# Kernel optimization log

Hardware: AMD Instinct MI355X
Metric: run time of the kernel (lower is better)

## Reference

```python
import jax, jax.numpy as jnp
import numpy as np

LOSS_WEIGHT = 1.0  # init kwarg
B = 16   # number of segments
S = 2048 # points per segment (uniform; offsets are cumulative multiples of S)


def setup_inputs() -> dict:
    key = jax.random.key(0)
    k1, k2, k3, k4 = jax.random.split(key, 4)
    coord = jax.random.normal(k1, (B * S, 3), dtype=jnp.float32)
    coord_transformed = jax.random.normal(k2, (B * S, 3), dtype=jnp.float32)
    R = jax.random.normal(k3, (B, 3, 3), dtype=jnp.float32)
    t = jax.random.normal(k4, (B, 3), dtype=jnp.float32)
    offset = (jnp.arange(B, dtype=jnp.int64) + 1) * S          # cumulative end offsets
    offset_trans = (jnp.arange(B, dtype=jnp.int64) + 1) * S
    return {"coord": coord, "coord_transformed": coord_transformed,
            "R": R, "t": t, "offset": offset, "offset_trans": offset_trans}


def reference(coord, coord_transformed, R, t, offset, offset_trans):
    # Uniform segments: reshape ragged-by-offset layout to [B, S, 3].
    b = R.shape[0]
    s = coord.shape[0] // b
    src = coord.reshape(b, s, 3)
    tgt = coord_transformed.reshape(b, -1, 3)
    # Per-segment rigid transform: (Ri @ src.T).T + ti
    src_t = jnp.einsum('bij,bnj->bni', R, src) + t[:, None, :]
    # Squared pairwise distances [B, S, S] (min of dist then square == min of sq-dist).
    d2 = (jnp.sum(src_t * src_t, axis=-1)[:, :, None]
          + jnp.sum(tgt * tgt, axis=-1)[:, None, :]
          - 2.0 * jnp.einsum('bnd,bmd->bnm', src_t, tgt))
    nn_d2 = jnp.min(jnp.maximum(d2, 0.0), axis=2)  # [B, S] NN squared distance
    per_seg = jnp.mean(nn_d2, axis=1)              # reduction='mean' within segment
    loss = jnp.mean(per_seg)                       # reduction='mean' over segments
    return loss * LOSS_WEIGHT
```

## Files before the change

### kernel.cpp

```cpp
#include <hip/hip_runtime.h>
#include <math.h>


#define THREADS 512
#define NW 8
#define P 2
#define SRC_BLK 128

__global__ __launch_bounds__(THREADS)
void nn_full_kernel(const float* __restrict__ coord,
                    const float* __restrict__ coord_t,
                    const float* __restrict__ Rm,
                    const float* __restrict__ tv,
                    float* __restrict__ ws,
                    int S, int NSC) {
    extern __shared__ char smem_raw[];
    float4* tile = (float4*)smem_raw;
    float*  part = (float*)(smem_raw + (size_t)S * 16);
    float*  wsum = part + NW * 64 * P;

    const int tid  = threadIdx.x;
    const int bid  = blockIdx.x;
    const int b    = bid / NSC;
    const int sc   = bid - b * NSC;
    const int w    = tid >> 6;
    const int lane = tid & 63;

    {
        const float* tb = coord_t + (size_t)b * S * 3;
        for (int base = tid * 4; base < S; base += THREADS * 4) {
            const float4* g4 = reinterpret_cast<const float4*>(tb + (size_t)base * 3);
            const float4 q0 = g4[0], q1 = g4[1], q2 = g4[2];
            const float px[4] = {q0.x, q0.w, q1.z, q2.y};
            const float py[4] = {q0.y, q1.x, q1.w, q2.z};
            const float pz[4] = {q0.z, q1.y, q2.x, q2.w};
            #pragma unroll
            for (int k = 0; k < 4; ++k) {
                const float x = px[k], y = py[k], z = pz[k];
                tile[base + k] = make_float4(-2.f*x, -2.f*y, -2.f*z,
                                             x*x + y*y + z*z);
            }
        }
    }

    const float* Rb = Rm + (size_t)b * 9;
    const float r00=Rb[0], r01=Rb[1], r02=Rb[2];
    const float r10=Rb[3], r11=Rb[4], r12=Rb[5];
    const float r20=Rb[6], r21=Rb[7], r22=Rb[8];
    const float t0=tv[3*b], t1=tv[3*b+1], t2=tv[3*b+2];

    float TX[P], TY[P], TZ[P], SN[P], best[P];
    {
        const float* sp = coord + ((size_t)b * S + (size_t)sc * SRC_BLK + lane * P) * 3;
        #pragma unroll
        for (int j = 0; j < P; ++j) {
            const float x = sp[3*j], y = sp[3*j+1], z = sp[3*j+2];
            const float sx = __builtin_fmaf(r00,x,__builtin_fmaf(r01,y,__builtin_fmaf(r02,z,t0)));
            const float sy = __builtin_fmaf(r10,x,__builtin_fmaf(r11,y,__builtin_fmaf(r12,z,t1)));
            const float sz = __builtin_fmaf(r20,x,__builtin_fmaf(r21,y,__builtin_fmaf(r22,z,t2)));
            TX[j]=sx; TY[j]=sy; TZ[j]=sz;
            SN[j]=sx*sx + sy*sy + sz*sz;
            best[j] = 3.0e38f;
        }
    }

    __syncthreads();

    const int mPer  = S / NW;
    const int mbase = w * mPer;
    #pragma unroll 2
    for (int it = 0; it < mPer / 4; ++it) {
        const float4 p0 = tile[mbase + 4*it + 0];
        const float4 p1 = tile[mbase + 4*it + 1];
        const float4 p2 = tile[mbase + 4*it + 2];
        const float4 p3 = tile[mbase + 4*it + 3];
        #pragma unroll
        for (int j = 0; j < P; ++j) {
            const float v0 = __builtin_fmaf(p0.x,TX[j],__builtin_fmaf(p0.y,TY[j],__builtin_fmaf(p0.z,TZ[j],p0.w)));
            const float v1 = __builtin_fmaf(p1.x,TX[j],__builtin_fmaf(p1.y,TY[j],__builtin_fmaf(p1.z,TZ[j],p1.w)));
            const float v2 = __builtin_fmaf(p2.x,TX[j],__builtin_fmaf(p2.y,TY[j],__builtin_fmaf(p2.z,TZ[j],p2.w)));
            const float v3 = __builtin_fmaf(p3.x,TX[j],__builtin_fmaf(p3.y,TY[j],__builtin_fmaf(p3.z,TZ[j],p3.w)));
            best[j] = fminf(fminf(best[j], v0), v1);
            best[j] = fminf(fminf(best[j], v2), v3);
        }
    }

    #pragma unroll
    for (int j = 0; j < P; ++j)
        part[(w * 64 + lane) * P + j] = best[j] + SN[j];
    __syncthreads();

    float v = 0.0f;
    if (tid < SRC_BLK) {
        float mn = part[tid];
        #pragma unroll
        for (int ww = 1; ww < NW; ++ww)
            mn = fminf(mn, part[ww * SRC_BLK + tid]);
        v = fmaxf(mn, 0.0f);
    }
    if (tid < 128) {
        #pragma unroll
        for (int off = 32; off > 0; off >>= 1) v += __shfl_down(v, off, 64);
        if ((tid & 63) == 0) wsum[tid >> 6] = v;
    }
    __syncthreads();
    if (tid == 0) ws[bid] = wsum[0] + wsum[1];
}

__global__ __launch_bounds__(256)
void final_kernel(const float* __restrict__ partial, int n,
                  float* __restrict__ out, float scale) {
    float v = (threadIdx.x < n) ? partial[threadIdx.x] : 0.0f;
    #pragma unroll
    for (int off = 32; off > 0; off >>= 1) v += __shfl_down(v, off, 64);
    __shared__ float sm[4];
    if ((threadIdx.x & 63) == 0) sm[threadIdx.x >> 6] = v;
    __syncthreads();
    if (threadIdx.x == 0) out[0] = (sm[0] + sm[1] + sm[2] + sm[3]) * scale;
}

extern "C" void kernel_launch(void* const* d_in, const int* in_sizes, int n_in,
                              void* d_out, int out_size, void* d_ws, size_t ws_size,
                              hipStream_t stream) {
    const float* coord   = (const float*)d_in[0];
    const float* coord_t = (const float*)d_in[1];
    const float* Rm      = (const float*)d_in[2];
    const float* tv      = (const float*)d_in[3];

    const int B = in_sizes[2] / 9;
    const int S = in_sizes[0] / (3 * B);
    const int NSC = S / SRC_BLK;
    const int nblk = B * NSC;

    float* ws  = (float*)d_ws;
    float* out = (float*)d_out;

    const size_t smem = (size_t)S * 16 + NW * 64 * P * 4 + 2 * 4;

    nn_full_kernel<<<nblk, THREADS, smem, stream>>>(
        coord, coord_t, Rm, tv, ws, S, NSC);

    final_kernel<<<1, 256, 0, stream>>>(
        ws, nblk, out, 1.0f / ((float)B * (float)S));
}
```

Before: 14.32 us.

## Split target set across two blocks and raise per-thread source points

Each block now scans only half of the segment's target points (TSPLIT=2) and handles 256 source points with 4 per thread instead of 128 with 2. Every block writes per-source partial minima to workspace, and a single 1024-thread combine kernel takes the min of the two halves, clamps at zero and sums. The aim is more register reuse of each shared-memory tile load and a smaller static shared tile. The cost is an extra global round trip of 2·B·S floats through one serial reduction block, and the tile is now hardcoded at 1024 entries, which ties it to S≤2048.

```diff
diff --git a/kernel.cpp b/kernel.cpp
--- a/kernel.cpp
+++ b/kernel.cpp
@@ -4,31 +4,33 @@
 
 #define THREADS 512
 #define NW 8
-#define P 2
-#define SRC_BLK 128
+#define P 4
+#define SRC_BLK 256
+#define TSPLIT 2
 
 __global__ __launch_bounds__(THREADS)
-void nn_full_kernel(const float* __restrict__ coord,
+void nn_half_kernel(const float* __restrict__ coord,
                     const float* __restrict__ coord_t,
                     const float* __restrict__ Rm,
                     const float* __restrict__ tv,
-                    float* __restrict__ ws,
-                    int S, int NSC) {
-    extern __shared__ char smem_raw[];
-    float4* tile = (float4*)smem_raw;
-    float*  part = (float*)(smem_raw + (size_t)S * 16);
-    float*  wsum = part + NW * 64 * P;
+                    float* __restrict__ slice_min,
+                    int S, int NSC, int BS) {
+    __shared__ float4 tile[1024];
+    __shared__ float  part[NW * SRC_BLK];
 
     const int tid  = threadIdx.x;
     const int bid  = blockIdx.x;
-    const int b    = bid / NSC;
-    const int sc   = bid - b * NSC;
+    const int b    = bid / (NSC * TSPLIT);
+    const int rem  = bid - b * (NSC * TSPLIT);
+    const int sc   = rem / TSPLIT;
+    const int ts   = rem - sc * TSPLIT;
     const int w    = tid >> 6;
     const int lane = tid & 63;
+    const int halfS = S / TSPLIT;
 
     {
-        const float* tb = coord_t + (size_t)b * S * 3;
-        for (int base = tid * 4; base < S; base += THREADS * 4) {
+        const float* tb = coord_t + ((size_t)b * S + (size_t)ts * halfS) * 3;
+        for (int base = tid * 4; base < halfS; base += THREADS * 4) {
             const float4* g4 = reinterpret_cast<const float4*>(tb + (size_t)base * 3);
             const float4 q0 = g4[0], q1 = g4[1], q2 = g4[2];
             const float px[4] = {q0.x, q0.w, q1.z, q2.y};
@@ -51,10 +53,14 @@
 
     float TX[P], TY[P], TZ[P], SN[P], best[P];
     {
-        const float* sp = coord + ((size_t)b * S + (size_t)sc * SRC_BLK + lane * P) * 3;
+        const float4* g4 = reinterpret_cast<const float4*>(
+            coord + ((size_t)b * S + (size_t)sc * SRC_BLK + lane * P) * 3);
+        const float4 q0 = g4[0], q1 = g4[1], q2 = g4[2];
+        const float f[12] = {q0.x,q0.y,q0.z,q0.w, q1.x,q1.y,q1.z,q1.w,
+                             q2.x,q2.y,q2.z,q2.w};
         #pragma unroll
         for (int j = 0; j < P; ++j) {
-            const float x = sp[3*j], y = sp[3*j+1], z = sp[3*j+2];
+            const float x = f[3*j], y = f[3*j+1], z = f[3*j+2];
             const float sx = __builtin_fmaf(r00,x,__builtin_fmaf(r01,y,__builtin_fmaf(r02,z,t0)));
             const float sy = __builtin_fmaf(r10,x,__builtin_fmaf(r11,y,__builtin_fmaf(r12,z,t1)));
             const float sz = __builtin_fmaf(r20,x,__builtin_fmaf(r21,y,__builtin_fmaf(r22,z,t2)));
@@ -66,10 +72,9 @@
 
     __syncthreads();
 
-    const int mPer  = S / NW;
-    const int mbase = w * mPer;
+    const int mbase = w * (halfS / NW);
     #pragma unroll 2
-    for (int it = 0; it < mPer / 4; ++it) {
+    for (int it = 0; it < (halfS / NW) / 4; ++it) {
         const float4 p0 = tile[mbase + 4*it + 0];
         const float4 p1 = tile[mbase + 4*it + 1];
         const float4 p2 = tile[mbase + 4*it + 2];
@@ -87,36 +92,46 @@
 
     #pragma unroll
     for (int j = 0; j < P; ++j)
-        part[(w * 64 + lane) * P + j] = best[j] + SN[j];
+        part[w * SRC_BLK + lane * P + j] = best[j] + SN[j];
     __syncthreads();
 
-    float v = 0.0f;
     if (tid < SRC_BLK) {
         float mn = part[tid];
         #pragma unroll
         for (int ww = 1; ww < NW; ++ww)
             mn = fminf(mn, part[ww * SRC_BLK + tid]);
-        v = fmaxf(mn, 0.0f);
+        slice_min[(size_t)ts * BS + (size_t)b * S + (size_t)sc * SRC_BLK + tid] = mn;
     }
-    if (tid < 128) {
-        #pragma unroll
-        for (int off = 32; off > 0; off >>= 1) v += __shfl_down(v, off, 64);
-        if ((tid & 63) == 0) wsum[tid >> 6] = v;
-    }
-    __syncthreads();
-    if (tid == 0) ws[bid] = wsum[0] + wsum[1];
 }
 
-__global__ __launch_bounds__(256)
-void final_kernel(const float* __restrict__ partial, int n,
-                  float* __restrict__ out, float scale) {
-    float v = (threadIdx.x < n) ? partial[threadIdx.x] : 0.0f;
+__global__ __launch_bounds__(1024)
+void combine_final_kernel(const float* __restrict__ slice_min,
+                          float* __restrict__ out, int BS, float scale) {
+    __shared__ float sm[16];
+    const float4* s0 = reinterpret_cast<const float4*>(slice_min);
+    const float4* s1 = reinterpret_cast<const float4*>(slice_min + BS);
+    const int n4 = BS / 4;
+
+    float acc = 0.0f;
+    for (int i = threadIdx.x; i < n4; i += 1024) {
+        const float4 a = s0[i];
+        const float4 c = s1[i];
+        const float m0 = fmaxf(fminf(a.x, c.x), 0.0f);
+        const float m1 = fmaxf(fminf(a.y, c.y), 0.0f);
+        const float m2 = fmaxf(fminf(a.z, c.z), 0.0f);
+        const float m3 = fmaxf(fminf(a.w, c.w), 0.0f);
+        acc += (m0 + m1) + (m2 + m3);
+    }
     #pragma unroll
-    for (int off = 32; off > 0; off >>= 1) v += __shfl_down(v, off, 64);
-    __shared__ float sm[4];
-    if ((threadIdx.x & 63) == 0) sm[threadIdx.x >> 6] = v;
+    for (int off = 32; off > 0; off >>= 1) acc += __shfl_down(acc, off, 64);
+    if ((threadIdx.x & 63) == 0) sm[threadIdx.x >> 6] = acc;
     __syncthreads();
-    if (threadIdx.x == 0) out[0] = (sm[0] + sm[1] + sm[2] + sm[3]) * scale;
+    if (threadIdx.x == 0) {
+        float tot = 0.0f;
+        #pragma unroll
+        for (int i = 0; i < 16; ++i) tot += sm[i];
+        out[0] = tot * scale;
+    }
 }
 
 extern "C" void kernel_launch(void* const* d_in, const int* in_sizes, int n_in,
@@ -129,17 +144,16 @@
 
     const int B = in_sizes[2] / 9;
     const int S = in_sizes[0] / (3 * B);
+    const int BS = B * S;
     const int NSC = S / SRC_BLK;
-    const int nblk = B * NSC;
+    const int nblk = B * NSC * TSPLIT;
 
-    float* ws  = (float*)d_ws;
+    float* slice_min = (float*)d_ws;
     float* out = (float*)d_out;
 
-    const size_t smem = (size_t)S * 16 + NW * 64 * P * 4 + 2 * 4;
+    nn_half_kernel<<<nblk, THREADS, 0, stream>>>(
+        coord, coord_t, Rm, tv, slice_min, S, NSC, BS);
 
-    nn_full_kernel<<<nblk, THREADS, smem, stream>>>(
-        coord, coord_t, Rm, tv, ws, S, NSC);
-
-    final_kernel<<<1, 256, 0, stream>>>(
-        ws, nblk, out, 1.0f / ((float)B * (float)S));
+    combine_final_kernel<<<1, 1024, 0, stream>>>(
+        slice_min, out, BS, 1.0f / (float)BS);
 }
```

After: 16.39 us. 14.5% more time.

## Stream target points via wave-uniform scalar loads instead of LDS tile

Applied to the files above, without the earlier changes.

Removes the shared-memory staging of the target segment and the barrier that follows it. Each wave now reads its slice of target points directly from global memory with a wave-uniform address (readfirstlane), so the loads can become scalar loads, and it computes the target norms inline. The -2 factor is folded into the source coordinates instead. This saves LDS traffic and the sync, and the smaller LDS footprint may raise occupancy. In exchange every block recomputes the target norms, which adds ALU work per pair, and the scalar load path must keep pace with the math.

```diff
diff --git a/kernel.cpp b/kernel.cpp
--- a/kernel.cpp
+++ b/kernel.cpp
@@ -6,6 +6,7 @@
 #define NW 8
 #define P 2
 #define SRC_BLK 128
+#define CHUNK 16
 
 __global__ __launch_bounds__(THREADS)
 void nn_full_kernel(const float* __restrict__ coord,
@@ -14,34 +15,14 @@
                     const float* __restrict__ tv,
                     float* __restrict__ ws,
                     int S, int NSC) {
-    extern __shared__ char smem_raw[];
-    float4* tile = (float4*)smem_raw;
-    float*  part = (float*)(smem_raw + (size_t)S * 16);
-    float*  wsum = part + NW * 64 * P;
+    __shared__ float part[NW * 64 * P];
+    __shared__ float wsum[2];
 
     const int tid  = threadIdx.x;
     const int bid  = blockIdx.x;
     const int b    = bid / NSC;
     const int sc   = bid - b * NSC;
-    const int w    = tid >> 6;
     const int lane = tid & 63;
-
-    {
-        const float* tb = coord_t + (size_t)b * S * 3;
-        for (int base = tid * 4; base < S; base += THREADS * 4) {
-            const float4* g4 = reinterpret_cast<const float4*>(tb + (size_t)base * 3);
-            const float4 q0 = g4[0], q1 = g4[1], q2 = g4[2];
-            const float px[4] = {q0.x, q0.w, q1.z, q2.y};
-            const float py[4] = {q0.y, q1.x, q1.w, q2.z};
-            const float pz[4] = {q0.z, q1.y, q2.x, q2.w};
-            #pragma unroll
-            for (int k = 0; k < 4; ++k) {
-                const float x = px[k], y = py[k], z = pz[k];
-                tile[base + k] = make_float4(-2.f*x, -2.f*y, -2.f*z,
-                                             x*x + y*y + z*z);
-            }
-        }
-    }
 
     const float* Rb = Rm + (size_t)b * 9;
     const float r00=Rb[0], r01=Rb[1], r02=Rb[2];
@@ -49,7 +30,7 @@
     const float r20=Rb[6], r21=Rb[7], r22=Rb[8];
     const float t0=tv[3*b], t1=tv[3*b+1], t2=tv[3*b+2];
 
-    float TX[P], TY[P], TZ[P], SN[P], best[P];
+    float TXp[P], TYp[P], TZp[P], SN[P], best[P];
     {
         const float* sp = coord + ((size_t)b * S + (size_t)sc * SRC_BLK + lane * P) * 3;
         #pragma unroll
@@ -58,36 +39,50 @@
             const float sx = __builtin_fmaf(r00,x,__builtin_fmaf(r01,y,__builtin_fmaf(r02,z,t0)));
             const float sy = __builtin_fmaf(r10,x,__builtin_fmaf(r11,y,__builtin_fmaf(r12,z,t1)));
             const float sz = __builtin_fmaf(r20,x,__builtin_fmaf(r21,y,__builtin_fmaf(r22,z,t2)));
-            TX[j]=sx; TY[j]=sy; TZ[j]=sz;
-            SN[j]=sx*sx + sy*sy + sz*sz;
+            TXp[j] = -2.0f * sx;  TYp[j] = -2.0f * sy;  TZp[j] = -2.0f * sz;
+            SN[j]  = sx*sx + sy*sy + sz*sz;
             best[j] = 3.0e38f;
         }
     }
 
-    __syncthreads();
+    const int w_u = __builtin_amdgcn_readfirstlane(tid >> 6);
+    const int mPer = S / NW;
+    const float* tb = coord_t + ((size_t)b * S + (size_t)w_u * mPer) * 3;
 
-    const int mPer  = S / NW;
-    const int mbase = w * mPer;
-    #pragma unroll 2
-    for (int it = 0; it < mPer / 4; ++it) {
-        const float4 p0 = tile[mbase + 4*it + 0];
-        const float4 p1 = tile[mbase + 4*it + 1];
-        const float4 p2 = tile[mbase + 4*it + 2];
-        const float4 p3 = tile[mbase + 4*it + 3];
+    for (int c = 0; c < mPer / CHUNK; ++c) {
+        const float* cb = tb + c * (CHUNK * 3);
+        float f[CHUNK * 3];
         #pragma unroll
-        for (int j = 0; j < P; ++j) {
-            const float v0 = __builtin_fmaf(p0.x,TX[j],__builtin_fmaf(p0.y,TY[j],__builtin_fmaf(p0.z,TZ[j],p0.w)));
-            const float v1 = __builtin_fmaf(p1.x,TX[j],__builtin_fmaf(p1.y,TY[j],__builtin_fmaf(p1.z,TZ[j],p1.w)));
-            const float v2 = __builtin_fmaf(p2.x,TX[j],__builtin_fmaf(p2.y,TY[j],__builtin_fmaf(p2.z,TZ[j],p2.w)));
-            const float v3 = __builtin_fmaf(p3.x,TX[j],__builtin_fmaf(p3.y,TY[j],__builtin_fmaf(p3.z,TZ[j],p3.w)));
-            best[j] = fminf(fminf(best[j], v0), v1);
-            best[j] = fminf(fminf(best[j], v2), v3);
+        for (int k = 0; k < CHUNK * 3; ++k) f[k] = cb[k];
+
+        #pragma unroll
+        for (int t = 0; t < CHUNK; t += 2) {
+            const float tx0 = f[3*t+0], ty0 = f[3*t+1], tz0 = f[3*t+2];
+            const float tx1 = f[3*t+3], ty1 = f[3*t+4], tz1 = f[3*t+5];
+            const float tn0 = __builtin_fmaf(tz0, tz0,
+                              __builtin_fmaf(ty0, ty0, tx0 * tx0));
+            const float tn1 = __builtin_fmaf(tz1, tz1,
+                              __builtin_fmaf(ty1, ty1, tx1 * tx1));
+            const float a00 = __builtin_fmaf(tx0, TXp[0],
+                              __builtin_fmaf(ty0, TYp[0],
+                              __builtin_fmaf(tz0, TZp[0], tn0)));
+            const float a01 = __builtin_fmaf(tx1, TXp[0],
+                              __builtin_fmaf(ty1, TYp[0],
+                              __builtin_fmaf(tz1, TZp[0], tn1)));
+            const float a10 = __builtin_fmaf(tx0, TXp[1],
+                              __builtin_fmaf(ty0, TYp[1],
+                              __builtin_fmaf(tz0, TZp[1], tn0)));
+            const float a11 = __builtin_fmaf(tx1, TXp[1],
+                              __builtin_fmaf(ty1, TYp[1],
+                              __builtin_fmaf(tz1, TZp[1], tn1)));
+            best[0] = fminf(fminf(best[0], a00), a01);
+            best[1] = fminf(fminf(best[1], a10), a11);
         }
     }
 
     #pragma unroll
     for (int j = 0; j < P; ++j)
-        part[(w * 64 + lane) * P + j] = best[j] + SN[j];
+        part[tid * P + j] = best[j] + SN[j];
     __syncthreads();
 
     float v = 0.0f;
@@ -135,9 +130,7 @@
     float* ws  = (float*)d_ws;
     float* out = (float*)d_out;
 
-    const size_t smem = (size_t)S * 16 + NW * 64 * P * 4 + 2 * 4;
-
-    nn_full_kernel<<<nblk, THREADS, smem, stream>>>(
+    nn_full_kernel<<<nblk, THREADS, 0, stream>>>(
         coord, coord_t, Rm, tv, ws, S, NSC);
 
     final_kernel<<<1, 256, 0, stream>>>(
```

After: 18.20 us. 27.1% more time.

## Compute pairwise distance dot products with fp16 MFMA using hi/lo split

Applied to the files above, without the earlier changes.

Replaces the scalar FMA inner loop with 32x32x16 f16 MFMA instructions. Source coordinates are split into high and low fp16 parts, and the target norm is packed into the B fragment so a single matrix multiply yields -2·s·t + |t|². The min is then taken over MFMA outputs and reduced with shuffles and LDS. This moves the O(S²) work onto the matrix cores, at the cost of precision: target coordinates are only fp16 and shared memory is now fixed at 2048 entries.

```diff
diff --git a/kernel.cpp b/kernel.cpp
--- a/kernel.cpp
+++ b/kernel.cpp
@@ -4,20 +4,31 @@
 
 #define THREADS 512
 #define NW 8
-#define P 2
 #define SRC_BLK 128
+#define PART_STRIDE 18
+
+typedef __attribute__((ext_vector_type(8))) _Float16 half8;
+typedef __attribute__((ext_vector_type(16))) float f32x16;
+
+__device__ __forceinline__ unsigned short f16b(float x) {
+    _Float16 hv = (_Float16)x;
+    return __builtin_bit_cast(unsigned short, hv);
+}
+__device__ __forceinline__ float f16tof(unsigned short u) {
+    return (float)__builtin_bit_cast(_Float16, u);
+}
 
 __global__ __launch_bounds__(THREADS)
-void nn_full_kernel(const float* __restrict__ coord,
+void nn_mfma_kernel(const float* __restrict__ coord,
                     const float* __restrict__ coord_t,
                     const float* __restrict__ Rm,
                     const float* __restrict__ tv,
                     float* __restrict__ ws,
                     int S, int NSC) {
-    extern __shared__ char smem_raw[];
-    float4* tile = (float4*)smem_raw;
-    float*  part = (float*)(smem_raw + (size_t)S * 16);
-    float*  wsum = part + NW * 64 * P;
+    __shared__ uint4 Bfrag[2048];
+    __shared__ float part[128 * PART_STRIDE];
+    __shared__ float SN_lds[128];
+    __shared__ float wsum[2];
 
     const int tid  = threadIdx.x;
     const int bid  = blockIdx.x;
@@ -25,83 +36,96 @@
     const int sc   = bid - b * NSC;
     const int w    = tid >> 6;
     const int lane = tid & 63;
+    const int col  = lane & 31;
+    const int kh   = lane >> 5;
+    const int wsrc = w >> 1;
+    const int h    = w & 1;
 
     {
         const float* tb = coord_t + (size_t)b * S * 3;
-        for (int base = tid * 4; base < S; base += THREADS * 4) {
-            const float4* g4 = reinterpret_cast<const float4*>(tb + (size_t)base * 3);
-            const float4 q0 = g4[0], q1 = g4[1], q2 = g4[2];
-            const float px[4] = {q0.x, q0.w, q1.z, q2.y};
-            const float py[4] = {q0.y, q1.x, q1.w, q2.z};
-            const float pz[4] = {q0.z, q1.y, q2.x, q2.w};
-            #pragma unroll
-            for (int k = 0; k < 4; ++k) {
-                const float x = px[k], y = py[k], z = pz[k];
-                tile[base + k] = make_float4(-2.f*x, -2.f*y, -2.f*z,
-                                             x*x + y*y + z*z);
-            }
+        for (int g = tid; g < S; g += THREADS) {
+            const float tx = tb[3*g], ty = tb[3*g+1], tz = tb[3*g+2];
+            const float TN = __builtin_fmaf(tz, tz, __builtin_fmaf(ty, ty, tx*tx));
+            const unsigned uhx = f16b(-2.f*tx), uhy = f16b(-2.f*ty), uhz = f16b(-2.f*tz);
+            const unsigned TNh = f16b(TN);
+            const unsigned TNl = f16b(TN - f16tof((unsigned short)TNh));
+            uint4 wv;
+            wv.x = uhx | (uhy << 16);
+            wv.y = uhz | (uhx << 16);
+            wv.z = uhy | (uhz << 16);
+            wv.w = TNh | (TNl << 16);
+            Bfrag[g] = wv;
         }
     }
 
-    const float* Rb = Rm + (size_t)b * 9;
-    const float r00=Rb[0], r01=Rb[1], r02=Rb[2];
-    const float r10=Rb[3], r11=Rb[4], r12=Rb[5];
-    const float r20=Rb[6], r21=Rb[7], r22=Rb[8];
-    const float t0=tv[3*b], t1=tv[3*b+1], t2=tv[3*b+2];
+    half8 afrag;
+    #pragma unroll
+    for (int i = 0; i < 8; ++i) afrag[i] = (_Float16)0.0f;
+    {
+        const float* Rb = Rm + (size_t)b * 9;
+        const float r00=Rb[0], r01=Rb[1], r02=Rb[2];
+        const float r10=Rb[3], r11=Rb[4], r12=Rb[5];
+        const float r20=Rb[6], r21=Rb[7], r22=Rb[8];
+        const float t0=tv[3*b], t1=tv[3*b+1], t2=tv[3*b+2];
 
-    float TX[P], TY[P], TZ[P], SN[P], best[P];
-    {
-        const float* sp = coord + ((size_t)b * S + (size_t)sc * SRC_BLK + lane * P) * 3;
-        #pragma unroll
-        for (int j = 0; j < P; ++j) {
-            const float x = sp[3*j], y = sp[3*j+1], z = sp[3*j+2];
-            const float sx = __builtin_fmaf(r00,x,__builtin_fmaf(r01,y,__builtin_fmaf(r02,z,t0)));
-            const float sy = __builtin_fmaf(r10,x,__builtin_fmaf(r11,y,__builtin_fmaf(r12,z,t1)));
-            const float sz = __builtin_fmaf(r20,x,__builtin_fmaf(r21,y,__builtin_fmaf(r22,z,t2)));
-            TX[j]=sx; TY[j]=sy; TZ[j]=sz;
-            SN[j]=sx*sx + sy*sy + sz*sz;
-            best[j] = 3.0e38f;
+        const float* sp = coord + ((size_t)b*S + (size_t)sc*SRC_BLK + wsrc*32 + col) * 3;
+        const float x = sp[0], y = sp[1], z = sp[2];
+        const float sx = __builtin_fmaf(r00,x,__builtin_fmaf(r01,y,__builtin_fmaf(r02,z,t0)));
+        const float sy = __builtin_fmaf(r10,x,__builtin_fmaf(r11,y,__builtin_fmaf(r12,z,t1)));
+        const float sz = __builtin_fmaf(r20,x,__builtin_fmaf(r21,y,__builtin_fmaf(r22,z,t2)));
+        const float SN = __builtin_fmaf(sz, sz, __builtin_fmaf(sy, sy, sx*sx));
+        if (h == 0 && kh == 0) SN_lds[wsrc*32 + col] = SN;
+        if (kh == 0) {
+            const _Float16 shx = (_Float16)sx, shy = (_Float16)sy, shz = (_Float16)sz;
+            const _Float16 slx = (_Float16)(sx - (float)shx);
+            const _Float16 sly = (_Float16)(sy - (float)shy);
+            const _Float16 slz = (_Float16)(sz - (float)shz);
+            afrag[0] = shx; afrag[1] = shy; afrag[2] = shz;
+            afrag[3] = slx; afrag[4] = sly; afrag[5] = slz;
+            afrag[6] = (_Float16)1.0f; afrag[7] = (_Float16)1.0f;
         }
     }
 
     __syncthreads();
 
-    const int mPer  = S / NW;
-    const int mbase = w * mPer;
-    #pragma unroll 2
-    for (int it = 0; it < mPer / 4; ++it) {
-        const float4 p0 = tile[mbase + 4*it + 0];
-        const float4 p1 = tile[mbase + 4*it + 1];
-        const float4 p2 = tile[mbase + 4*it + 2];
-        const float4 p3 = tile[mbase + 4*it + 3];
+    f32x16 zf, mn;
+    #pragma unroll
+    for (int r = 0; r < 16; ++r) { zf[r] = 0.0f; mn[r] = 1e30f; }
+
+    const uint4* Bp = &Bfrag[h*1024 + col];
+    const int nit = S >> 7;
+    for (int it = 0; it < nit; ++it) {
+        const half8 b0 = *reinterpret_cast<const half8*>(Bp + it*64);
+        const half8 b1 = *reinterpret_cast<const half8*>(Bp + it*64 + 32);
+        const f32x16 aA = __builtin_amdgcn_mfma_f32_32x32x16_f16(afrag, b0, zf, 0, 0, 0);
+        const f32x16 aB = __builtin_amdgcn_mfma_f32_32x32x16_f16(afrag, b1, zf, 0, 0, 0);
         #pragma unroll
-        for (int j = 0; j < P; ++j) {
-            const float v0 = __builtin_fmaf(p0.x,TX[j],__builtin_fmaf(p0.y,TY[j],__builtin_fmaf(p0.z,TZ[j],p0.w)));
-            const float v1 = __builtin_fmaf(p1.x,TX[j],__builtin_fmaf(p1.y,TY[j],__builtin_fmaf(p1.z,TZ[j],p1.w)));
-            const float v2 = __builtin_fmaf(p2.x,TX[j],__builtin_fmaf(p2.y,TY[j],__builtin_fmaf(p2.z,TZ[j],p2.w)));
-            const float v3 = __builtin_fmaf(p3.x,TX[j],__builtin_fmaf(p3.y,TY[j],__builtin_fmaf(p3.z,TZ[j],p3.w)));
-            best[j] = fminf(fminf(best[j], v0), v1);
-            best[j] = fminf(fminf(best[j], v2), v3);
-        }
+        for (int r = 0; r < 16; ++r)
+            mn[r] = fminf(fminf(mn[r], aA[r]), aB[r]);
     }
 
     #pragma unroll
-    for (int j = 0; j < P; ++j)
-        part[(w * 64 + lane) * P + j] = best[j] + SN[j];
+    for (int r = 0; r < 16; ++r) {
+        float v = mn[r];
+        v = fminf(v, __shfl_xor(v, 1, 64));
+        v = fminf(v, __shfl_xor(v, 2, 64));
+        if ((col & 3) == 0) {
+            const int row = (r & 3) + 8*(r >> 2) + 4*kh;
+            part[(wsrc*32 + row)*PART_STRIDE + h*8 + (col >> 2)] = v;
+        }
+    }
     __syncthreads();
 
-    float v = 0.0f;
-    if (tid < SRC_BLK) {
-        float mn = part[tid];
+    float acc = 0.0f;
+    if (tid < 128) {
+        const float* pp = &part[tid * PART_STRIDE];
+        float m = pp[0];
         #pragma unroll
-        for (int ww = 1; ww < NW; ++ww)
-            mn = fminf(mn, part[ww * SRC_BLK + tid]);
-        v = fmaxf(mn, 0.0f);
-    }
-    if (tid < 128) {
+        for (int j = 1; j < 16; ++j) m = fminf(m, pp[j]);
+        acc = fmaxf(SN_lds[tid] + m, 0.0f);
         #pragma unroll
-        for (int off = 32; off > 0; off >>= 1) v += __shfl_down(v, off, 64);
-        if ((tid & 63) == 0) wsum[tid >> 6] = v;
+        for (int off = 32; off > 0; off >>= 1) acc += __shfl_down(acc, off, 64);
+        if ((tid & 63) == 0) wsum[tid >> 6] = acc;
     }
     __syncthreads();
     if (tid == 0) ws[bid] = wsum[0] + wsum[1];
@@ -135,9 +159,7 @@
     float* ws  = (float*)d_ws;
     float* out = (float*)d_out;
 
-    const size_t smem = (size_t)S * 16 + NW * 64 * P * 4 + 2 * 4;
-
-    nn_full_kernel<<<nblk, THREADS, smem, stream>>>(
+    nn_mfma_kernel<<<nblk, THREADS, 0, stream>>>(
         coord, coord_t, Rm, tv, ws, S, NSC);
 
     final_kernel<<<1, 256, 0, stream>>>(
```

After: 12.25 us. 1.17x faster.
